# Kernel tuning notes

Hardware: AMD Instinct MI355X
Metric: run time of the kernel (lower is better)

## Reference

```python
import jax, jax.numpy as jnp
import numpy as np

B, T, V, H, O = 256, 1024, 128, 128, 2  # batch, max_len, input_size, hidden, n_outputs


def setup_inputs() -> dict:
    key = jax.random.key(0)
    ks = jax.random.split(key, 9)
    # ragged one-hot sequences: symbol 0 is the pad symbol
    lengths = jax.random.randint(ks[0], (B,), 1, T + 1)
    symbols = jax.random.randint(ks[1], (B, T), 1, V)  # real symbols in [1, V)
    t_idx = jnp.arange(T)[None, :]
    symbols = jnp.where(t_idx < lengths[:, None], symbols, 0)  # pad tail with symbol 0
    x = jax.nn.one_hot(symbols, V, dtype=jnp.float32)  # [B, T, V]
    # RNN params (torch nn.RNN layout: W_ih [H, V-1], W_hh [H, H])
    s = 1.0 / np.sqrt(H)
    W_ih = jax.random.uniform(ks[2], (H, V - 1), minval=-s, maxval=s)
    W_hh = jax.random.uniform(ks[3], (H, H), minval=-s, maxval=s)
    b_ih = jax.random.uniform(ks[4], (H,), minval=-s, maxval=s)
    b_hh = jax.random.uniform(ks[5], (H,), minval=-s, maxval=s)
    # dense head: Linear(H, O)
    W_out = jax.random.uniform(ks[6], (O, H), minval=-s, maxval=s)
    b_out = jax.random.uniform(ks[7], (O,), minval=-s, maxval=s)
    return {"x": x, "W_ih": W_ih, "W_hh": W_hh, "b_ih": b_ih,
            "b_hh": b_hh, "W_out": W_out, "b_out": b_out}


def reference(x, W_ih, W_hh, b_ih, b_hh, W_out, b_out):
    Bk, Tk, Vk = x.shape
    # unpad: length = first timestep whose argmax is the pad symbol (index 0)
    is_pad = jnp.argmax(x, axis=-1) == 0  # [B, T]
    length = jnp.where(is_pad.any(-1), jnp.argmax(is_pad, axis=-1), Tk)  # [B]
    active = jnp.arange(Tk)[None, :] < length[:, None]  # [B, T]
    feats = x[..., 1:]  # strip pad column -> [B, T, V-1]
    # precompute input projection for all timesteps (streaming part)
    pre = jnp.einsum('btf,hf->bth', feats, W_ih) + b_ih + b_hh  # [B, T, H]

    def step(h, inp):
        pre_t, act_t = inp  # [B, H], [B]
        h_new = jnp.tanh(pre_t + h @ W_hh.T)
        h = jnp.where(act_t[:, None], h_new, h)  # freeze hidden past each seq's length
        return h, None

    h0 = jnp.zeros((Bk, W_hh.shape[0]), dtype=x.dtype)
    h_last, _ = jax.lax.scan(step, h0, (pre.transpose(1, 0, 2), active.T))
    fed = jax.nn.softmax(h_last @ W_out.T + b_out, axis=-1)  # [B, O]
    hidden = h_last[None]  # [1, B, H], matches torch stacked layer hidden
    return fed, hidden
```

## Files before the change

kernel.cpp:

```cpp
#include <hip/hip_runtime.h>
#include <stdint.h>

#define Bsz   256
#define Tlen  1024
#define Vocab 128
#define Hdim  128
#define NTHR  512
#define CH    36
#define WTN   ((Vocab - 1) * Hdim)

__device__ __forceinline__ float tanh_fast(float x) {
    float e = __builtin_amdgcn_exp2f(x * 2.885390081777927f);
    return 1.0f - 2.0f * __builtin_amdgcn_rcpf(e + 1.0f);
}

__device__ __forceinline__ float dpp_xor1(float s) {
    return __int_as_float(__builtin_amdgcn_mov_dpp(__float_as_int(s), 0xB1, 0xF, 0xF, true));
}
__device__ __forceinline__ float dpp_xor2(float s) {
    return __int_as_float(__builtin_amdgcn_mov_dpp(__float_as_int(s), 0x4E, 0xF, 0xF, true));
}

__global__ __launch_bounds__(256) void transpose_kernel(
    const float* __restrict__ W_ih, float* __restrict__ wt)
{
    int idx = blockIdx.x * 256 + threadIdx.x;
    if (idx < WTN) {
        int h = idx / (Vocab - 1);
        int f = idx - h * (Vocab - 1);
        wt[f * Hdim + h] = W_ih[idx];
    }
}

__global__ __launch_bounds__(NTHR, 2) void rnn_kernel(
    const float* __restrict__ x, const float* __restrict__ wt,
    const float* __restrict__ W_hh,
    const float* __restrict__ b_ih, const float* __restrict__ b_hh,
    const float* __restrict__ W_out, const float* __restrict__ b_out,
    float* __restrict__ out)
{
    __shared__ float wt_s[WTN];
    __shared__ int   syms[Tlen];
    __shared__ float hbuf[2][4 * CH];
    __shared__ int   len_sh;

    const int tid  = threadIdx.x;
    const int b    = blockIdx.x;
    const int wave = tid >> 6;
    const int l    = tid & 63;
    const int i    = (wave << 4) + (l >> 2);
    const int q    = l & 3;

    if (tid == 0) len_sh = Tlen;
    if (tid < 2 * 4 * CH) ((float*)hbuf)[tid] = 0.0f;

    float w[32];
    {
        const float4* wrow = (const float4*)(W_hh + i * Hdim + q * 32);
        #pragma unroll
        for (int k = 0; k < 8; k++) {
            float4 t4 = wrow[k];
            w[4 * k + 0] = t4.x; w[4 * k + 1] = t4.y;
            w[4 * k + 2] = t4.z; w[4 * k + 3] = t4.w;
        }
    }
    const float bias = b_ih[i] + b_hh[i];

    {
        const float4* src = (const float4*)wt;
        float4* dst = (float4*)wt_s;
        for (int k = tid; k < WTN / 4; k += NTHR) dst[k] = src[k];
    }

    const float4* xb = (const float4*)(x + (size_t)b * Tlen * Vocab);
    for (int k = tid; k < (Tlen * Vocab) / 4; k += NTHR) {
        float4 v = xb[k];
        int c = -1;
        if      (v.x > 0.5f) c = 0;
        else if (v.y > 0.5f) c = 1;
        else if (v.z > 0.5f) c = 2;
        else if (v.w > 0.5f) c = 3;
        if (c >= 0) syms[k >> 5] = ((k & 31) << 2) + c;
    }
    __syncthreads();

    {
        int lm = Tlen;
        for (int k = tid; k < Tlen; k += NTHR)
            if (syms[k] == 0 && k < lm) lm = k;
        if (lm < Tlen) atomicMin(&len_sh, lm);
    }
    __syncthreads();
    const int len = len_sh;

    float pre_v = 0.0f, p_t1 = 0.0f;
    int   s_t2 = 1;
    if (len > 0) pre_v = wt_s[(syms[0] - 1) * Hdim + i];
    if (len > 1) p_t1  = wt_s[(syms[1] - 1) * Hdim + i];
    if (len > 2) s_t2  = syms[2];

    const int rdoff = q * CH;
    const int wroff = (i >> 5) * CH + (i & 31);
    for (int t = 0; t < len; t++) {
        #pragma unroll
        for (int k = 0; k < 32; k += 8)
            asm volatile("" : "+v"(w[k]), "+v"(w[k+1]), "+v"(w[k+2]), "+v"(w[k+3]),
                             "+v"(w[k+4]), "+v"(w[k+5]), "+v"(w[k+6]), "+v"(w[k+7]));

        float p_t2 = wt_s[(s_t2 - 1) * Hdim + i];
        int   s_t3 = (t + 3 < len) ? syms[t + 3] : 1;

        const float4* hsrc = (const float4*)(hbuf[t & 1] + rdoff);
        float ax = 0.0f, ay = 0.0f, az = 0.0f, aw = 0.0f;
        #pragma unroll
        for (int k = 0; k < 8; k++) {
            float4 hv = hsrc[k];
            ax = fmaf(w[4 * k + 0], hv.x, ax);
            ay = fmaf(w[4 * k + 1], hv.y, ay);
            az = fmaf(w[4 * k + 2], hv.z, az);
            aw = fmaf(w[4 * k + 3], hv.w, aw);
        }
        float sum = (ax + ay) + (az + aw);
        sum += dpp_xor1(sum);
        sum += dpp_xor2(sum);
        float hn = tanh_fast(sum + pre_v + bias);
        if (q == 0) hbuf[(t + 1) & 1][wroff] = hn;
        pre_v = p_t1; p_t1 = p_t2; s_t2 = s_t3;
        __syncthreads();
    }

    const float* hf = hbuf[len & 1];
    if (tid < Hdim)
        out[2 * Bsz + b * Hdim + tid] = hf[(tid >> 5) * CH + (tid & 31)];
    if (tid < 64) {
        float h0 = hf[(tid >> 5) * CH + (tid & 31)];
        int j = tid + 64;
        float h1 = hf[(j >> 5) * CH + (j & 31)];
        float p0 = W_out[tid] * h0 + W_out[64 + tid] * h1;
        float p1 = W_out[128 + tid] * h0 + W_out[192 + tid] * h1;
        #pragma unroll
        for (int off = 32; off > 0; off >>= 1) {
            p0 += __shfl_down(p0, off, 64);
            p1 += __shfl_down(p1, off, 64);
        }
        if (tid == 0) {
            float l0 = p0 + b_out[0], l1 = p1 + b_out[1];
            float m  = fmaxf(l0, l1);
            float e0 = __expf(l0 - m), e1 = __expf(l1 - m);
            float d  = e0 + e1;
            out[b * 2 + 0] = e0 / d;
            out[b * 2 + 1] = e1 / d;
        }
    }
}

extern "C" void kernel_launch(void* const* d_in, const int* in_sizes, int n_in,
                              void* d_out, int out_size, void* d_ws, size_t ws_size,
                              hipStream_t stream) {
    const float* x     = (const float*)d_in[0];
    const float* W_ih  = (const float*)d_in[1];
    const float* W_hh  = (const float*)d_in[2];
    const float* b_ih  = (const float*)d_in[3];
    const float* b_hh  = (const float*)d_in[4];
    const float* W_out = (const float*)d_in[5];
    const float* b_out = (const float*)d_in[6];
    float* out = (float*)d_out;

    float* wt = (float*)d_ws;

    const int NTRN = (WTN + 255) / 256;
    transpose_kernel<<<NTRN, 256, 0, stream>>>(W_ih, wt);
    rnn_kernel<<<Bsz, NTHR, 0, stream>>>(x, wt, W_hh, b_ih, b_hh, W_out, b_out, out);
}
```

Before: 535.3 us.

## Halve RNN block threads with each thread computing four hidden rows

Shrinks the recurrent block from 512 to 256 threads. Each group of 8 lanes now handles 4 hidden units, with each lane holding 64 W_hh weights and reading a 16-element slice of h. Partial sums are reduced with DPP and a shuffle, and the h buffer uses a new padded stride. The aim is to cut barrier cost per timestep by using fewer waves, at the price of more register pressure, an extra cross-lane shuffle, and one block per CU.

```diff
diff --git a/kernel.cpp b/kernel.cpp
--- a/kernel.cpp
+++ b/kernel.cpp
@@ -5,9 +5,12 @@
 #define Tlen  1024
 #define Vocab 128
 #define Hdim  128
-#define NTHR  512
-#define CH    36
+#define NTHR  256
 #define WTN   ((Vocab - 1) * Hdim)
+
+#define HSTR  20
+#define HBUFN (8 * HSTR)
+#define HADDR(e) ((((e) >> 4) * HSTR) + ((e) & 15))
 
 __device__ __forceinline__ float tanh_fast(float x) {
     float e = __builtin_amdgcn_exp2f(x * 2.885390081777927f);
@@ -32,7 +35,7 @@
     }
 }
 
-__global__ __launch_bounds__(NTHR, 2) void rnn_kernel(
+__global__ __launch_bounds__(NTHR, 1) void rnn_kernel(
     const float* __restrict__ x, const float* __restrict__ wt,
     const float* __restrict__ W_hh,
     const float* __restrict__ b_ih, const float* __restrict__ b_hh,
@@ -41,30 +44,32 @@
 {
     __shared__ float wt_s[WTN];
     __shared__ int   syms[Tlen];
-    __shared__ float hbuf[2][4 * CH];
+    __shared__ __align__(16) float hbuf[2][HBUFN];
     __shared__ int   len_sh;
 
-    const int tid  = threadIdx.x;
-    const int b    = blockIdx.x;
-    const int wave = tid >> 6;
-    const int l    = tid & 63;
-    const int i    = (wave << 4) + (l >> 2);
-    const int q    = l & 3;
+    const int tid = threadIdx.x;
+    const int b   = blockIdx.x;
+    const int wv  = tid >> 6;
+    const int l   = tid & 63;
+    const int G   = (wv << 3) + (l >> 3);
+    const int j   = l & 7;
+    const int eo  = 4 * G + (j & 3);
 
     if (tid == 0) len_sh = Tlen;
-    if (tid < 2 * 4 * CH) ((float*)hbuf)[tid] = 0.0f;
+    for (int k = tid; k < 2 * HBUFN; k += NTHR) ((float*)hbuf)[k] = 0.0f;
 
-    float w[32];
-    {
-        const float4* wrow = (const float4*)(W_hh + i * Hdim + q * 32);
+    float w[64];
+    #pragma unroll
+    for (int r = 0; r < 4; r++) {
+        const float4* wrow = (const float4*)(W_hh + (4 * G + r) * Hdim + 16 * j);
         #pragma unroll
-        for (int k = 0; k < 8; k++) {
-            float4 t4 = wrow[k];
-            w[4 * k + 0] = t4.x; w[4 * k + 1] = t4.y;
-            w[4 * k + 2] = t4.z; w[4 * k + 3] = t4.w;
+        for (int k4 = 0; k4 < 4; k4++) {
+            float4 t4 = wrow[k4];
+            w[r * 16 + 4 * k4 + 0] = t4.x; w[r * 16 + 4 * k4 + 1] = t4.y;
+            w[r * 16 + 4 * k4 + 2] = t4.z; w[r * 16 + 4 * k4 + 3] = t4.w;
         }
     }
-    const float bias = b_ih[i] + b_hh[i];
+    const float bias = b_ih[eo] + b_hh[eo];
 
     {
         const float4* src = (const float4*)wt;
@@ -95,47 +100,59 @@
 
     float pre_v = 0.0f, p_t1 = 0.0f;
     int   s_t2 = 1;
-    if (len > 0) pre_v = wt_s[(syms[0] - 1) * Hdim + i];
-    if (len > 1) p_t1  = wt_s[(syms[1] - 1) * Hdim + i];
+    if (len > 0) pre_v = wt_s[(syms[0] - 1) * Hdim + eo];
+    if (len > 1) p_t1  = wt_s[(syms[1] - 1) * Hdim + eo];
     if (len > 2) s_t2  = syms[2];
 
-    const int rdoff = q * CH;
-    const int wroff = (i >> 5) * CH + (i & 31);
+    const float4* rd0 = (const float4*)(hbuf[0] + j * HSTR);
+    const float4* rd1 = (const float4*)(hbuf[1] + j * HSTR);
+    const int waddr = HADDR(eo);
+
     for (int t = 0; t < len; t++) {
         #pragma unroll
-        for (int k = 0; k < 32; k += 8)
+        for (int k = 0; k < 64; k += 8)
             asm volatile("" : "+v"(w[k]), "+v"(w[k+1]), "+v"(w[k+2]), "+v"(w[k+3]),
                              "+v"(w[k+4]), "+v"(w[k+5]), "+v"(w[k+6]), "+v"(w[k+7]));
 
-        float p_t2 = wt_s[(s_t2 - 1) * Hdim + i];
+        float p_t2 = wt_s[(s_t2 - 1) * Hdim + eo];
         int   s_t3 = (t + 3 < len) ? syms[t + 3] : 1;
 
-        const float4* hsrc = (const float4*)(hbuf[t & 1] + rdoff);
-        float ax = 0.0f, ay = 0.0f, az = 0.0f, aw = 0.0f;
+        const float4* hsrc = (t & 1) ? rd1 : rd0;
+        float4 h0 = hsrc[0], h1 = hsrc[1], h2 = hsrc[2], h3 = hsrc[3];
+        float hv[16] = {h0.x,h0.y,h0.z,h0.w, h1.x,h1.y,h1.z,h1.w,
+                        h2.x,h2.y,h2.z,h2.w, h3.x,h3.y,h3.z,h3.w};
+
+        float s[4];
         #pragma unroll
-        for (int k = 0; k < 8; k++) {
-            float4 hv = hsrc[k];
-            ax = fmaf(w[4 * k + 0], hv.x, ax);
-            ay = fmaf(w[4 * k + 1], hv.y, ay);
-            az = fmaf(w[4 * k + 2], hv.z, az);
-            aw = fmaf(w[4 * k + 3], hv.w, aw);
+        for (int r = 0; r < 4; r++) {
+            float a0 = 0.0f, a1 = 0.0f;
+            #pragma unroll
+            for (int k = 0; k < 8; k++) {
+                a0 = fmaf(w[r * 16 + k],     hv[k],     a0);
+                a1 = fmaf(w[r * 16 + 8 + k], hv[8 + k], a1);
+            }
+            s[r] = a0 + a1;
         }
-        float sum = (ax + ay) + (az + aw);
-        sum += dpp_xor1(sum);
-        sum += dpp_xor2(sum);
-        float hn = tanh_fast(sum + pre_v + bias);
-        if (q == 0) hbuf[(t + 1) & 1][wroff] = hn;
+        #pragma unroll
+        for (int r = 0; r < 4; r++) {
+            s[r] += dpp_xor1(s[r]);
+            s[r] += dpp_xor2(s[r]);
+            s[r] += __shfl_xor(s[r], 4, 64);
+        }
+        int rs = j & 3;
+        float s_own = (rs == 0) ? s[0] : (rs == 1) ? s[1] : (rs == 2) ? s[2] : s[3];
+        float hn = tanh_fast(s_own + pre_v + bias);
+        if (j < 4) hbuf[(t + 1) & 1][waddr] = hn;
         pre_v = p_t1; p_t1 = p_t2; s_t2 = s_t3;
         __syncthreads();
     }
 
     const float* hf = hbuf[len & 1];
     if (tid < Hdim)
-        out[2 * Bsz + b * Hdim + tid] = hf[(tid >> 5) * CH + (tid & 31)];
+        out[2 * Bsz + b * Hdim + tid] = hf[HADDR(tid)];
     if (tid < 64) {
-        float h0 = hf[(tid >> 5) * CH + (tid & 31)];
-        int j = tid + 64;
-        float h1 = hf[(j >> 5) * CH + (j & 31)];
+        float h0 = hf[HADDR(tid)];
+        float h1 = hf[HADDR(tid + 64)];
         float p0 = W_out[tid] * h0 + W_out[64 + tid] * h1;
         float p1 = W_out[128 + tid] * h0 + W_out[192 + tid] * h1;
         #pragma unroll
```

Measured after the change: 688.5 us. +28.6%, slower.

## Store hidden state and W_hh in fp16 and use packed dot2 for recurrence

Applied to the files above, without the earlier changes.

The recurrent matvec now keeps W_hh as packed fp16 pairs in registers and the hidden state as fp16 in shared memory, using v_dot2 instructions with fp32 accumulation. Work is remapped so each group of 8 lanes computes two hidden units over 16-element slices, with a three-stage DPP reduction and one lane writing a packed pair. The aim is to halve the shared-memory read traffic and the FMA count on the serial per-timestep critical path. The cost is fp16 rounding of the hidden state and weights, which accumulates across up to 1024 steps and may exceed tolerance; the final hidden output is also returned from fp16.

```diff
diff --git a/kernel.cpp b/kernel.cpp
--- a/kernel.cpp
+++ b/kernel.cpp
@@ -6,8 +6,12 @@
 #define Vocab 128
 #define Hdim  128
 #define NTHR  512
-#define CH    36
 #define WTN   ((Vocab - 1) * Hdim)
+
+typedef _Float16 half2_t __attribute__((ext_vector_type(2)));
+
+#define HCHB  48
+#define HBUFI (8 * HCHB / 4)
 
 __device__ __forceinline__ float tanh_fast(float x) {
     float e = __builtin_amdgcn_exp2f(x * 2.885390081777927f);
@@ -19,6 +23,9 @@
 }
 __device__ __forceinline__ float dpp_xor2(float s) {
     return __int_as_float(__builtin_amdgcn_mov_dpp(__float_as_int(s), 0x4E, 0xF, 0xF, true));
+}
+__device__ __forceinline__ float dpp_hm(float s) {
+    return __int_as_float(__builtin_amdgcn_mov_dpp(__float_as_int(s), 0x141, 0xF, 0xF, true));
 }
 
 __global__ __launch_bounds__(256) void transpose_kernel(
@@ -41,30 +48,30 @@
 {
     __shared__ float wt_s[WTN];
     __shared__ int   syms[Tlen];
-    __shared__ float hbuf[2][4 * CH];
+    __shared__ __align__(16) int hbuf[2][HBUFI];
     __shared__ int   len_sh;
 
-    const int tid  = threadIdx.x;
-    const int b    = blockIdx.x;
-    const int wave = tid >> 6;
-    const int l    = tid & 63;
-    const int i    = (wave << 4) + (l >> 2);
-    const int q    = l & 3;
+    const int tid = threadIdx.x;
+    const int b   = blockIdx.x;
+    const int g   = tid >> 3;
+    const int j   = tid & 7;
 
     if (tid == 0) len_sh = Tlen;
-    if (tid < 2 * 4 * CH) ((float*)hbuf)[tid] = 0.0f;
+    for (int k = tid; k < 2 * HBUFI; k += NTHR) ((int*)hbuf)[k] = 0;
 
-    float w[32];
-    {
-        const float4* wrow = (const float4*)(W_hh + i * Hdim + q * 32);
+    int wp[16];
+    #pragma unroll
+    for (int r = 0; r < 2; r++) {
+        const float4* wrow = (const float4*)(W_hh + (2 * g + r) * Hdim + 16 * j);
         #pragma unroll
-        for (int k = 0; k < 8; k++) {
-            float4 t4 = wrow[k];
-            w[4 * k + 0] = t4.x; w[4 * k + 1] = t4.y;
-            w[4 * k + 2] = t4.z; w[4 * k + 3] = t4.w;
+        for (int q4 = 0; q4 < 4; q4++) {
+            float4 t4 = wrow[q4];
+            wp[r * 8 + q4 * 2 + 0] = __builtin_bit_cast(int, __builtin_amdgcn_cvt_pkrtz(t4.x, t4.y));
+            wp[r * 8 + q4 * 2 + 1] = __builtin_bit_cast(int, __builtin_amdgcn_cvt_pkrtz(t4.z, t4.w));
         }
     }
-    const float bias = b_ih[i] + b_hh[i];
+    const float bias0 = b_ih[2 * g]     + b_hh[2 * g];
+    const float bias1 = b_ih[2 * g + 1] + b_hh[2 * g + 1];
 
     {
         const float4* src = (const float4*)wt;
@@ -93,49 +100,60 @@
     __syncthreads();
     const int len = len_sh;
 
-    float pre_v = 0.0f, p_t1 = 0.0f;
-    int   s_t2 = 1;
-    if (len > 0) pre_v = wt_s[(syms[0] - 1) * Hdim + i];
-    if (len > 1) p_t1  = wt_s[(syms[1] - 1) * Hdim + i];
+    const float2* wt2 = (const float2*)wt_s;
+    float2 pre_v = {0.0f, 0.0f}, p_t1 = {0.0f, 0.0f};
+    int s_t2 = 1;
+    if (len > 0) pre_v = wt2[(syms[0] - 1) * 64 + g];
+    if (len > 1) p_t1  = wt2[(syms[1] - 1) * 64 + g];
     if (len > 2) s_t2  = syms[2];
 
-    const int rdoff = q * CH;
-    const int wroff = (i >> 5) * CH + (i & 31);
+    const char* hb0 = (const char*)hbuf[0];
+    const char* hb1 = (const char*)hbuf[1];
+    const int roff = j * HCHB;
+    const int woff = (g >> 3) * HCHB + ((2 * g) & 15) * 2;
+
     for (int t = 0; t < len; t++) {
         #pragma unroll
-        for (int k = 0; k < 32; k += 8)
-            asm volatile("" : "+v"(w[k]), "+v"(w[k+1]), "+v"(w[k+2]), "+v"(w[k+3]),
-                             "+v"(w[k+4]), "+v"(w[k+5]), "+v"(w[k+6]), "+v"(w[k+7]));
+        for (int k = 0; k < 16; k += 8)
+            asm volatile("" : "+v"(wp[k]), "+v"(wp[k+1]), "+v"(wp[k+2]), "+v"(wp[k+3]),
+                             "+v"(wp[k+4]), "+v"(wp[k+5]), "+v"(wp[k+6]), "+v"(wp[k+7]));
 
-        float p_t2 = wt_s[(s_t2 - 1) * Hdim + i];
+        float2 p_t2 = wt2[(s_t2 - 1) * 64 + g];
         int   s_t3 = (t + 3 < len) ? syms[t + 3] : 1;
 
-        const float4* hsrc = (const float4*)(hbuf[t & 1] + rdoff);
-        float ax = 0.0f, ay = 0.0f, az = 0.0f, aw = 0.0f;
+        const char* hb = (t & 1) ? hb1 : hb0;
+        uint4 r0 = *(const uint4*)(hb + roff);
+        uint4 r1 = *(const uint4*)(hb + roff + 16);
+        unsigned hr[8] = {r0.x, r0.y, r0.z, r0.w, r1.x, r1.y, r1.z, r1.w};
+
+        float a0 = 0.0f, a1 = 0.0f;
         #pragma unroll
-        for (int k = 0; k < 8; k++) {
-            float4 hv = hsrc[k];
-            ax = fmaf(w[4 * k + 0], hv.x, ax);
-            ay = fmaf(w[4 * k + 1], hv.y, ay);
-            az = fmaf(w[4 * k + 2], hv.z, az);
-            aw = fmaf(w[4 * k + 3], hv.w, aw);
+        for (int p = 0; p < 8; p++) {
+            half2_t hh = __builtin_bit_cast(half2_t, hr[p]);
+            a0 = __builtin_amdgcn_fdot2(hh, __builtin_bit_cast(half2_t, wp[p]),     a0, false);
+            a1 = __builtin_amdgcn_fdot2(hh, __builtin_bit_cast(half2_t, wp[8 + p]), a1, false);
         }
-        float sum = (ax + ay) + (az + aw);
-        sum += dpp_xor1(sum);
-        sum += dpp_xor2(sum);
-        float hn = tanh_fast(sum + pre_v + bias);
-        if (q == 0) hbuf[(t + 1) & 1][wroff] = hn;
+        a0 += dpp_xor1(a0); a1 += dpp_xor1(a1);
+        a0 += dpp_xor2(a0); a1 += dpp_xor2(a1);
+        a0 += dpp_hm(a0);   a1 += dpp_hm(a1);
+
+        if (j == 0) {
+            float h0 = tanh_fast(a0 + pre_v.x + bias0);
+            float h1 = tanh_fast(a1 + pre_v.y + bias1);
+            int pk = __builtin_bit_cast(int, __builtin_amdgcn_cvt_pkrtz(h0, h1));
+            *(int*)(((char*)hbuf[(t + 1) & 1]) + woff) = pk;
+        }
         pre_v = p_t1; p_t1 = p_t2; s_t2 = s_t3;
         __syncthreads();
     }
 
-    const float* hf = hbuf[len & 1];
+    const _Float16* hf = (const _Float16*)hbuf[len & 1];
+    #define HGET(e) ((float)hf[((e) >> 4) * 24 + ((e) & 15)])
     if (tid < Hdim)
-        out[2 * Bsz + b * Hdim + tid] = hf[(tid >> 5) * CH + (tid & 31)];
+        out[2 * Bsz + b * Hdim + tid] = HGET(tid);
     if (tid < 64) {
-        float h0 = hf[(tid >> 5) * CH + (tid & 31)];
-        int j = tid + 64;
-        float h1 = hf[(j >> 5) * CH + (j & 31)];
+        float h0 = HGET(tid);
+        float h1 = HGET(tid + 64);
         float p0 = W_out[tid] * h0 + W_out[64 + tid] * h1;
         float p1 = W_out[128 + tid] * h0 + W_out[192 + tid] * h1;
         #pragma unroll
@@ -152,6 +170,7 @@
             out[b * 2 + 1] = e1 / d;
         }
     }
+    #undef HGET
 }
 
 extern "C" void kernel_launch(void* const* d_in, const int* in_sizes, int n_in,
```

New measurement: 527.6 us. About the same (-1.4%).
